# Performance work log

Hardware: AMD Instinct MI355X
Metric: run time of the kernel (lower is better)

The kernel has to match this reference:

```python
import jax, jax.numpy as jnp
import numpy as np

MARGIN = 0.3


def _pairwise_dist(x):
    # Exact euclidean cdist; same math as torch.cdist's non-mm mode:
    # sqrt(sum_k (x_i[k]-x_j[k])^2) == sqrt(|x_i|^2 + |x_j|^2 - 2 x_i.x_j).
    sq = jnp.sum(x * x, axis=1)
    sqd = sq[:, None] + sq[None, :] - 2.0 * (x @ x.T)
    sqd = jnp.maximum(sqd, 0.0)
    # safe sqrt: zero distance (diagonal) -> dist 0 with zero grad, like torch
    safe = jnp.where(sqd > 0, sqd, 1.0)
    return jnp.where(sqd > 0, jnp.sqrt(safe), 0.0)


def setup_inputs() -> dict:
    key = jax.random.key(0)
    k1, k2 = jax.random.split(key)
    n, d, n_classes = 8192, 128, 64
    inputs = jax.random.normal(k1, (n, d), dtype=jnp.float32)
    targets = jax.random.randint(k2, (n,), 0, n_classes)
    return {"inputs": inputs, "targets": targets}


def reference(inputs, targets):
    dist = _pairwise_dist(inputs)  # (n, n)
    mask = targets[:, None] == targets[None, :]  # (n, n) same-label mask
    # hard positive: max distance among same-label (diag included, as in torch code)
    dist_ap = jnp.max(jnp.where(mask, dist, -jnp.inf), axis=1)  # (n,)
    # hard negative: min distance among different-label
    dist_an = jnp.min(jnp.where(mask, jnp.inf, dist), axis=1)  # (n,)
    # MarginRankingLoss with y=1: mean(relu(-(dist_an - dist_ap) + margin))
    loss = jnp.mean(jax.nn.relu(dist_ap - dist_an + MARGIN))
    return (loss, dist)
```

## Files before the change

kernel.cpp:

```cpp
#include <hip/hip_runtime.h>
#include <hip/hip_bf16.h>
#include <cstdint>
#include <cstddef>


#define NROWS 8192
#define DIMK  128
#define MARGIN 0.3f

typedef __bf16 bf16x8 __attribute__((ext_vector_type(8)));
typedef float  f32x4  __attribute__((ext_vector_type(4)));
typedef float  f32x2  __attribute__((ext_vector_type(2)));
typedef int    i32x4  __attribute__((ext_vector_type(4)));

__device__ __forceinline__ unsigned short f2bf(float f) {
    unsigned u = __float_as_uint(f);
    u += 0x7fffu + ((u >> 16) & 1u);
    return (unsigned short)(u >> 16);
}

__global__ __launch_bounds__(256) void prep_kernel(
    const float* __restrict__ X, unsigned short* __restrict__ Xb,
    float* __restrict__ sq, int* __restrict__ ap, int* __restrict__ an)
{
    const int t = blockIdx.x * 256 + threadIdx.x;
    if (t < NROWS) { ap[t] = 0; an[t] = 0x7f800000; }
    const int row  = t >> 6;
    const int lane = t & 63;
    const f32x2 v = *(const f32x2*)(X + (size_t)row * DIMK + lane * 2);
    const unsigned short b0 = f2bf(v[0]);
    const unsigned short b1 = f2bf(v[1]);
    *(unsigned*)(Xb + (size_t)row * DIMK + lane * 2) =
        (unsigned)b0 | ((unsigned)b1 << 16);
    const float f0 = __uint_as_float((unsigned)b0 << 16);
    const float f1 = __uint_as_float((unsigned)b1 << 16);
    float s = f0 * f0 + f1 * f1;
    #pragma unroll
    for (int off = 32; off; off >>= 1) s += __shfl_xor(s, off);
    if (lane == 0) sq[row] = s;
}

__device__ __forceinline__ void store_row_shifted(float* drow, f32x4 d4, int rc) {
    const float prev = __shfl_up(d4[3], 1);
    if (rc == 0) {
        drow[0] = d4[0];
        *(f32x2*)(drow + 1) = (f32x2){d4[1], d4[2]};
    } else {
        *(f32x4*)(drow + (rc << 2) - 1) = (f32x4){prev, d4[0], d4[1], d4[2]};
    }
    if (rc == 31)
        drow[127] = d4[3];
}

__global__ __launch_bounds__(256, 4) void dist_kernel(
    const unsigned short* __restrict__ Xb, const float* __restrict__ sq,
    const int* __restrict__ tgt, float* __restrict__ dist,
    int* __restrict__ ap, int* __restrict__ an)
{
    __shared__ __align__(16) char lds[32 * 1024];

    const int t = threadIdx.x;
    const int bm = blockIdx.x, bn = blockIdx.y;
    const int lane = t & 63, wave = t >> 6;
    const int wm = (wave >> 1) << 6;
    const int wn = (wave & 1) << 6;
    const int l15 = lane & 15, quad = lane >> 4;
    const int rbase = bm << 7, cbase = bn << 7;
    const float INF = __int_as_float(0x7f800000);

    f32x4 acc[4][4];
    #pragma unroll
    for (int mi = 0; mi < 4; mi++)
        #pragma unroll
        for (int ni = 0; ni < 4; ni++)
            acc[mi][ni] = (f32x4){0.f, 0.f, 0.f, 0.f};

    const unsigned short* Arow = Xb + (size_t)(rbase + wm + l15) * DIMK;
    const unsigned short* Brow = Xb + (size_t)(cbase + wn + l15) * DIMK;
    #pragma unroll
    for (int ks = 0; ks < 4; ks++) {
        const int kb = ks * 32 + quad * 8;
        bf16x8 af[4], bfr[4];
        #pragma unroll
        for (int mi = 0; mi < 4; mi++)
            af[mi] = *(const bf16x8*)(Arow + mi * 16 * DIMK + kb);
        #pragma unroll
        for (int ni = 0; ni < 4; ni++)
            bfr[ni] = *(const bf16x8*)(Brow + ni * 16 * DIMK + kb);
        #pragma unroll
        for (int mi = 0; mi < 4; mi++)
            #pragma unroll
            for (int ni = 0; ni < 4; ni++)
                acc[mi][ni] = __builtin_amdgcn_mfma_f32_16x16x32_bf16(
                    bfr[ni], af[mi], acc[mi][ni], 0, 0, 0);
    }

    int rg[4]; float sqr[4]; int trg[4];
    #pragma unroll
    for (int mi = 0; mi < 4; mi++) {
        rg[mi]  = rbase + wm + mi * 16 + l15;
        sqr[mi] = sq[rg[mi]];
        trg[mi] = tgt[rg[mi]];
    }
    float apv[4] = {-1.f, -1.f, -1.f, -1.f};
    float anv[4] = {INF, INF, INF, INF};

    #pragma unroll
    for (int ni = 0; ni < 4; ni++) {
        const int c0 = cbase + wn + ni * 16 + quad * 4;
        const f32x4 sqc = *(const f32x4*)(sq + c0);
        const i32x4 tc  = *(const i32x4*)(tgt + c0);
        #pragma unroll
        for (int mi = 0; mi < 4; mi++) {
            #pragma unroll
            for (int j = 0; j < 4; j++) {
                const float sqd = sqr[mi] + sqc[j] - 2.0f * acc[mi][ni][j];
                float d = sqd > 0.0f ? sqrtf(sqd) : 0.0f;
                if (rg[mi] == c0 + j) d = 0.0f;
                acc[mi][ni][j] = d;
                const bool same = (trg[mi] == tc[j]);
                apv[mi] = fmaxf(apv[mi], same ? d : -1.f);
                anv[mi] = fminf(anv[mi], same ? INF : d);
            }
        }
    }

    #pragma unroll
    for (int mi = 0; mi < 4; mi++) {
        apv[mi] = fmaxf(apv[mi], __shfl_xor(apv[mi], 16));
        apv[mi] = fmaxf(apv[mi], __shfl_xor(apv[mi], 32));
        anv[mi] = fminf(anv[mi], __shfl_xor(anv[mi], 16));
        anv[mi] = fminf(anv[mi], __shfl_xor(anv[mi], 32));
    }
    if (quad == 0) {
        #pragma unroll
        for (int mi = 0; mi < 4; mi++) {
            atomicMax(ap + rg[mi], __float_as_int(apv[mi]));
            atomicMin(an + rg[mi], __float_as_int(anv[mi]));
        }
    }

    const int rc = t & 31;
    const int w  = t >> 5;
    #pragma unroll
    for (int h = 0; h < 2; h++) {
        if (wm == h * 64) {
            #pragma unroll
            for (int mi = 0; mi < 4; mi++) {
                const int rl = mi * 16 + l15;
                const int sw = (rl & 7) << 4;
                #pragma unroll
                for (int ni = 0; ni < 4; ni++) {
                    const int cb = (wn + ni * 16 + quad * 4) << 2;
                    *(f32x4*)(lds + rl * 512 + (cb ^ sw)) = acc[mi][ni];
                }
            }
        }
        __syncthreads();
        #pragma unroll
        for (int it = 0; it < 8; it++) {
            const int r = it * 8 + w;
            const f32x4 d4 = *(const f32x4*)(
                lds + r * 512 + ((rc << 4) ^ ((r & 7) << 4)));
            const int rowg = rbase + h * 64 + r;
            store_row_shifted(dist + (size_t)rowg * NROWS + cbase, d4, rc);
        }
        __syncthreads();
    }
}

__global__ __launch_bounds__(256) void loss_kernel(
    const int* __restrict__ ap, const int* __restrict__ an,
    float* __restrict__ out)
{
    __shared__ float red[4];
    float s = 0.0f;
    for (int i = threadIdx.x; i < NROWS; i += 256) {
        const float v = __int_as_float(ap[i]) - __int_as_float(an[i]) + MARGIN;
        s += v > 0.0f ? v : 0.0f;
    }
    #pragma unroll
    for (int off = 32; off; off >>= 1) s += __shfl_xor(s, off);
    if ((threadIdx.x & 63) == 0) red[threadIdx.x >> 6] = s;
    __syncthreads();
    if (threadIdx.x == 0)
        out[0] = (red[0] + red[1] + red[2] + red[3]) * (1.0f / NROWS);
}

extern "C" void kernel_launch(void* const* d_in, const int* in_sizes, int n_in,
                              void* d_out, int out_size, void* d_ws, size_t ws_size,
                              hipStream_t stream)
{
    const float* X   = (const float*)d_in[0];
    const int*   tgt = (const int*)d_in[1];
    float*       out = (float*)d_out;

    unsigned short* Xb = (unsigned short*)d_ws;
    float* sq = (float*)((char*)d_ws + (size_t)NROWS * DIMK * 2);
    int*   ap = (int*)(sq + NROWS);
    int*   an = ap + NROWS;

    prep_kernel<<<(NROWS * 64) / 256, 256, 0, stream>>>(X, Xb, sq, ap, an);

    dim3 grid(64, 64);
    dist_kernel<<<grid, 256, 0, stream>>>(Xb, sq, tgt, out + 1, ap, an);

    loss_kernel<<<1, 256, 0, stream>>>(ap, an, out);
}
```

Baseline: 339.6 us.

## Replace global atomics with per-block partial max/min and parallel reduction

Drops the per-row global atomicMax/atomicMin from the distance kernel. Each block now merges its two column-waves through LDS and writes per-column-block partials to a 64xN workspace. A new multi-block reduce kernel combines the partials and sums the loss with one atomicAdd per block. The LDS barriers are also swapped for an inline lgkmcnt wait plus s_barrier. This trades atomic contention for extra workspace traffic and a larger reduce, with the output zeroed in the prep kernel.

Result: no change. 342.6 us (+0.9%).

```diff
diff --git a/kernel.cpp b/kernel.cpp
--- a/kernel.cpp
+++ b/kernel.cpp
@@ -13,6 +13,8 @@
 typedef float  f32x2  __attribute__((ext_vector_type(2)));
 typedef int    i32x4  __attribute__((ext_vector_type(4)));
 
+#define BAR_LDS() asm volatile("s_waitcnt lgkmcnt(0)\n\ts_barrier" ::: "memory")
+
 __device__ __forceinline__ unsigned short f2bf(float f) {
     unsigned u = __float_as_uint(f);
     u += 0x7fffu + ((u >> 16) & 1u);
@@ -21,10 +23,10 @@
 
 __global__ __launch_bounds__(256) void prep_kernel(
     const float* __restrict__ X, unsigned short* __restrict__ Xb,
-    float* __restrict__ sq, int* __restrict__ ap, int* __restrict__ an)
-{
+    float* __restrict__ sq, float* __restrict__ out)
+{
+    if (blockIdx.x == 0 && threadIdx.x == 0) out[0] = 0.0f;
     const int t = blockIdx.x * 256 + threadIdx.x;
-    if (t < NROWS) { ap[t] = 0; an[t] = 0x7f800000; }
     const int row  = t >> 6;
     const int lane = t & 63;
     const f32x2 v = *(const f32x2*)(X + (size_t)row * DIMK + lane * 2);
@@ -55,7 +57,7 @@
 __global__ __launch_bounds__(256, 4) void dist_kernel(
     const unsigned short* __restrict__ Xb, const float* __restrict__ sq,
     const int* __restrict__ tgt, float* __restrict__ dist,
-    int* __restrict__ ap, int* __restrict__ an)
+    float* __restrict__ app, float* __restrict__ anp)
 {
     __shared__ __align__(16) char lds[32 * 1024];
 
@@ -124,20 +126,12 @@
             }
         }
     }
-
     #pragma unroll
     for (int mi = 0; mi < 4; mi++) {
         apv[mi] = fmaxf(apv[mi], __shfl_xor(apv[mi], 16));
         apv[mi] = fmaxf(apv[mi], __shfl_xor(apv[mi], 32));
         anv[mi] = fminf(anv[mi], __shfl_xor(anv[mi], 16));
         anv[mi] = fminf(anv[mi], __shfl_xor(anv[mi], 32));
-    }
-    if (quad == 0) {
-        #pragma unroll
-        for (int mi = 0; mi < 4; mi++) {
-            atomicMax(ap + rg[mi], __float_as_int(apv[mi]));
-            atomicMin(an + rg[mi], __float_as_int(anv[mi]));
-        }
     }
 
     const int rc = t & 31;
@@ -156,7 +150,7 @@
                 }
             }
         }
-        __syncthreads();
+        BAR_LDS();
         #pragma unroll
         for (int it = 0; it < 8; it++) {
             const int r = it * 8 + w;
@@ -165,26 +159,50 @@
             const int rowg = rbase + h * 64 + r;
             store_row_shifted(dist + (size_t)rowg * NROWS + cbase, d4, rc);
         }
-        __syncthreads();
-    }
-}
-
-__global__ __launch_bounds__(256) void loss_kernel(
-    const int* __restrict__ ap, const int* __restrict__ an,
+        BAR_LDS();
+    }
+
+    float* apL = (float*)lds;
+    float* anL = apL + 128;
+    if (wn == 64 && quad == 0) {
+        #pragma unroll
+        for (int mi = 0; mi < 4; mi++) {
+            const int lr = wm + mi * 16 + l15;
+            apL[lr] = apv[mi];
+            anL[lr] = anv[mi];
+        }
+    }
+    BAR_LDS();
+    if (wn == 0 && quad == 0) {
+        #pragma unroll
+        for (int mi = 0; mi < 4; mi++) {
+            const int lr = wm + mi * 16 + l15;
+            app[(size_t)bn * NROWS + rbase + lr] = fmaxf(apv[mi], apL[lr]);
+            anp[(size_t)bn * NROWS + rbase + lr] = fminf(anv[mi], anL[lr]);
+        }
+    }
+}
+
+__global__ __launch_bounds__(256) void reduce_kernel(
+    const float* __restrict__ app, const float* __restrict__ anp,
     float* __restrict__ out)
 {
     __shared__ float red[4];
-    float s = 0.0f;
-    for (int i = threadIdx.x; i < NROWS; i += 256) {
-        const float v = __int_as_float(ap[i]) - __int_as_float(an[i]) + MARGIN;
-        s += v > 0.0f ? v : 0.0f;
-    }
+    const int r = blockIdx.x * 256 + threadIdx.x;
+    float ap = -1.0f, an = __int_as_float(0x7f800000);
+    #pragma unroll 8
+    for (int b = 0; b < 64; b++) {
+        ap = fmaxf(ap, app[(size_t)b * NROWS + r]);
+        an = fminf(an, anp[(size_t)b * NROWS + r]);
+    }
+    float v = ap - an + MARGIN;
+    float s = v > 0.0f ? v : 0.0f;
     #pragma unroll
     for (int off = 32; off; off >>= 1) s += __shfl_xor(s, off);
     if ((threadIdx.x & 63) == 0) red[threadIdx.x >> 6] = s;
     __syncthreads();
     if (threadIdx.x == 0)
-        out[0] = (red[0] + red[1] + red[2] + red[3]) * (1.0f / NROWS);
+        atomicAdd(out, (red[0] + red[1] + red[2] + red[3]) * (1.0f / NROWS));
 }
 
 extern "C" void kernel_launch(void* const* d_in, const int* in_sizes, int n_in,
@@ -196,14 +214,14 @@
     float*       out = (float*)d_out;
 
     unsigned short* Xb = (unsigned short*)d_ws;
-    float* sq = (float*)((char*)d_ws + (size_t)NROWS * DIMK * 2);
-    int*   ap = (int*)(sq + NROWS);
-    int*   an = ap + NROWS;
-
-    prep_kernel<<<(NROWS * 64) / 256, 256, 0, stream>>>(X, Xb, sq, ap, an);
+    float* sq  = (float*)((char*)d_ws + (size_t)NROWS * DIMK * 2);
+    float* app = sq + NROWS;
+    float* anp = app + (size_t)64 * NROWS;
+
+    prep_kernel<<<(NROWS * 64) / 256, 256, 0, stream>>>(X, Xb, sq, out);
 
     dim3 grid(64, 64);
-    dist_kernel<<<grid, 256, 0, stream>>>(Xb, sq, tgt, out + 1, ap, an);
-
-    loss_kernel<<<1, 256, 0, stream>>>(ap, an, out);
-}
+    dist_kernel<<<grid, 256, 0, stream>>>(Xb, sq, tgt, out + 1, app, anp);
+
+    reduce_kernel<<<NROWS / 256, 256, 0, stream>>>(app, anp, out);
+}
```
